# Kernel tuning notes

Measured on AMD Instinct MI355X. Metric: run time of the kernel, lower is better.

Reference implementation:

```python
import jax, jax.numpy as jnp
import numpy as np

NUM_HEADS = 12


def _build_mask(N, unseen_size, dtype):
    # Columns for the last `unseen_size` tokens are masked (-inf) for every
    # query row EXCEPT the diagonal entries in that block (each unseen token
    # may attend to itself). Matches the original Python-loop construction.
    idx = jnp.arange(N)
    col_unseen = idx[None, :] >= (N - unseen_size)
    off_diag = idx[:, None] != idx[None, :]
    return jnp.where(col_unseen & off_diag, -jnp.inf, jnp.asarray(0.0, dtype))


def reference(x, w_qkv, w_proj, b_proj, unseen_size):
    B, N, C = x.shape
    H = NUM_HEADS
    d = C // H
    scale = d ** -0.5
    # qkv: (B,N,3C) -> (3,B,H,N,d)
    qkv = (x @ w_qkv.T).reshape(B, N, 3, H, d).transpose(2, 0, 3, 1, 4)
    q, k, v = qkv[0], qkv[1], qkv[2]
    attn = jnp.einsum('bhqd,bhkd->bhqk', q, k) * scale
    attn = attn + _build_mask(N, unseen_size, attn.dtype)  # broadcast (N,N)
    attn = jax.nn.softmax(attn, axis=-1)
    out = jnp.einsum('bhqk,bhkd->bhqd', attn, v)
    out = out.transpose(0, 2, 1, 3).reshape(B, N, C)
    return out @ w_proj.T + b_proj


def setup_inputs() -> dict:
    key = jax.random.key(0)
    k1, k2, k3 = jax.random.split(key, 3)
    B, N, C = 2, 2048, 768
    x = jax.random.normal(k1, (B, N, C), dtype=jnp.float32)
    w_qkv = jax.random.normal(k2, (3 * C, C), dtype=jnp.float32) * (C ** -0.5)
    w_proj = jax.random.normal(k3, (C, C), dtype=jnp.float32) * (C ** -0.5)
    b_proj = jnp.zeros((C,), dtype=jnp.float32)
    return {"x": x, "w_qkv": w_qkv, "w_proj": w_proj, "b_proj": b_proj,
            "unseen_size": 512}
```

## Files before the change

kernel.cpp:

```cpp
#include <hip/hip_runtime.h>
#include <math.h>

#define NH 12
#define DH 64
#define NSEQ 2048
#define NB 2
#define CDIM 768
#define NVIS 1536

typedef _Float16 half8 __attribute__((ext_vector_type(8)));
typedef _Float16 half4 __attribute__((ext_vector_type(4)));
typedef float floatx4 __attribute__((ext_vector_type(4)));

static constexpr size_t SZ_X    = (size_t)NB*NSEQ*CDIM;
static constexpr size_t SZ_WQKV = (size_t)3*CDIM*CDIM;
static constexpr size_t SZ_WP   = (size_t)CDIM*CDIM;
static constexpr size_t SZ_HEAD = (size_t)NB*NH*NSEQ*DH;

__global__ __launch_bounds__(256) void convert_kernel(
    const float* __restrict__ x, const float* __restrict__ wqkv, const float* __restrict__ wp,
    _Float16* __restrict__ xb, _Float16* __restrict__ wqkvb, _Float16* __restrict__ wpb)
{
  size_t idx = ((size_t)blockIdx.x*256 + threadIdx.x)*4;
  const float* src; _Float16* dst; size_t off;
  if (idx < SZ_X)                        { src = x;    dst = xb;    off = idx; }
  else if (idx < SZ_X+SZ_WQKV)           { src = wqkv; dst = wqkvb; off = idx - SZ_X; }
  else if (idx < SZ_X+SZ_WQKV+SZ_WP)     { src = wp;   dst = wpb;   off = idx - SZ_X - SZ_WQKV; }
  else return;
  float4 v = *reinterpret_cast<const float4*>(src + off);
  _Float16 o[4] = {(_Float16)v.x,(_Float16)v.y,(_Float16)v.z,(_Float16)v.w};
  *reinterpret_cast<uint2*>(dst + off) = *reinterpret_cast<uint2*>(o);
}

template<int MODE>
__global__ __launch_bounds__(256) void gemm_bt(
    const _Float16* __restrict__ A, const _Float16* __restrict__ Bt,
    const float* __restrict__ bias,
    _Float16* __restrict__ qb, _Float16* __restrict__ kb, _Float16* __restrict__ vb,
    float* __restrict__ outp)
{
  constexpr int K = CDIM;
  constexpr int LDSST = 40;
  __shared__ _Float16 As[128*LDSST];
  __shared__ _Float16 Bs[128*LDSST];
  const int tid = threadIdx.x;
  const int lane = tid & 63, wid = tid >> 6;
  const int l15 = lane & 15, quad = lane >> 4;
  const int wm = (wid >> 1)*64, wn = (wid & 1)*64;
  const int tileN = blockIdx.x*128, tileM = blockIdx.y*128;
  const int srow = tid >> 2, scol = (tid & 3)*8;
  floatx4 acc[4][4] = {};
  for (int k0 = 0; k0 < K; k0 += 32) {
    uint4 a0 = *reinterpret_cast<const uint4*>(A  + (size_t)(tileM+srow)*K    + k0 + scol);
    uint4 a1 = *reinterpret_cast<const uint4*>(A  + (size_t)(tileM+64+srow)*K + k0 + scol);
    uint4 b0 = *reinterpret_cast<const uint4*>(Bt + (size_t)(tileN+srow)*K    + k0 + scol);
    uint4 b1 = *reinterpret_cast<const uint4*>(Bt + (size_t)(tileN+64+srow)*K + k0 + scol);
    __syncthreads();
    *reinterpret_cast<uint4*>(&As[srow*LDSST + scol])      = a0;
    *reinterpret_cast<uint4*>(&As[(64+srow)*LDSST + scol]) = a1;
    *reinterpret_cast<uint4*>(&Bs[srow*LDSST + scol])      = b0;
    *reinterpret_cast<uint4*>(&Bs[(64+srow)*LDSST + scol]) = b1;
    __syncthreads();
    half8 af[4], bfr[4];
    #pragma unroll
    for (int mi=0; mi<4; mi++)
      af[mi] = *reinterpret_cast<const half8*>(&As[(wm+mi*16+l15)*LDSST + quad*8]);
    #pragma unroll
    for (int ni=0; ni<4; ni++)
      bfr[ni] = *reinterpret_cast<const half8*>(&Bs[(wn+ni*16+l15)*LDSST + quad*8]);
    #pragma unroll
    for (int mi=0; mi<4; mi++)
      #pragma unroll
      for (int ni=0; ni<4; ni++)
        acc[mi][ni] = __builtin_amdgcn_mfma_f32_16x16x32_f16(af[mi], bfr[ni], acc[mi][ni], 0,0,0);
  }
  #pragma unroll
  for (int mi=0; mi<4; mi++)
    #pragma unroll
    for (int ni=0; ni<4; ni++) {
      int n = tileN + wn + ni*16 + l15;
      int m0 = tileM + wm + mi*16 + quad*4;
      if (MODE == 0) {
        int part = n / CDIM, rem = n - part*CDIM;
        int h = rem >> 6, dd = rem & 63;
        int b = m0 >> 11, i0 = m0 & 2047;
        if (part == 2) {
          half4 pk = {(_Float16)acc[mi][ni][0], (_Float16)acc[mi][ni][1],
                      (_Float16)acc[mi][ni][2], (_Float16)acc[mi][ni][3]};
          *reinterpret_cast<half4*>(&vb[(((size_t)b*NH + h)*DH + dd)*NSEQ + i0]) = pk;
        } else {
          _Float16* dst = part ? kb : qb;
          float sc = part ? 1.0f : 0.125f;
          #pragma unroll
          for (int r = 0; r < 4; r++)
            dst[(((size_t)b*NH + h)*NSEQ + i0 + r)*DH + dd] = (_Float16)(acc[mi][ni][r]*sc);
        }
      } else {
        #pragma unroll
        for (int r = 0; r < 4; r++)
          outp[(size_t)(m0 + r)*CDIM + n] = acc[mi][ni][r] + bias[n];
      }
    }
}

__global__ __launch_bounds__(256) void fa_kernel(
    const _Float16* __restrict__ qg, const _Float16* __restrict__ kg,
    const _Float16* __restrict__ vtg, _Float16* __restrict__ og)
{
  constexpr int LDK = 72;
  constexpr int LDP = 72;
  __shared__ _Float16 Ks[64*LDK];
  __shared__ _Float16 Vt[64*LDK];
  __shared__ _Float16 Ps[4][16*LDP];
  const int blk = blockIdx.x;
  const int idx = blk >> 3;
  const int bh = (blk & 7)*3 + (idx % 3);
  const int qbase = (idx / 3) * 64;
  const int tid = threadIdx.x;
  const int lane = tid & 63, w = tid >> 6;
  const int l15 = lane & 15, quad = lane >> 4;
  const _Float16* qptr = qg + ((size_t)bh*NSEQ + qbase + w*16 + l15)*DH + quad*8;
  half8 qf0 = *reinterpret_cast<const half8*>(qptr);
  half8 qf1 = *reinterpret_cast<const half8*>(qptr + 32);
  floatx4 o[4] = {};
  float lsum = 0.f;
  const int srow = tid >> 3, scol = (tid & 7)*8;
  const _Float16* kbp = kg  + (size_t)bh*NSEQ*DH;
  const _Float16* vbp = vtg + (size_t)bh*DH*NSEQ;
  for (int t = 0; t < 24; t++) {
    const int kvbase = t*64;
    const _Float16* kp = kbp + (size_t)(kvbase + srow)*DH + scol;
    const _Float16* vp = vbp + (size_t)srow*NSEQ + kvbase + scol;
    uint4 k0 = *reinterpret_cast<const uint4*>(kp);
    uint4 k1 = *reinterpret_cast<const uint4*>(kp + 32*DH);
    uint4 v0 = *reinterpret_cast<const uint4*>(vp);
    uint4 v1 = *reinterpret_cast<const uint4*>(vp + 32*NSEQ);
    __syncthreads();
    *reinterpret_cast<uint4*>(&Ks[srow*LDK + scol])      = k0;
    *reinterpret_cast<uint4*>(&Ks[(32+srow)*LDK + scol]) = k1;
    *reinterpret_cast<uint4*>(&Vt[srow*LDK + scol])      = v0;
    *reinterpret_cast<uint4*>(&Vt[(32+srow)*LDK + scol]) = v1;
    __syncthreads();
    #pragma unroll
    for (int f = 0; f < 4; f++) {
      half8 kf0 = *reinterpret_cast<const half8*>(&Ks[(f*16+l15)*LDK + quad*8]);
      half8 kf1 = *reinterpret_cast<const half8*>(&Ks[(f*16+l15)*LDK + 32 + quad*8]);
      floatx4 st = {};
      st = __builtin_amdgcn_mfma_f32_16x16x32_f16(kf0, qf0, st, 0,0,0);
      st = __builtin_amdgcn_mfma_f32_16x16x32_f16(kf1, qf1, st, 0,0,0);
      float e0 = __expf(st[0]), e1 = __expf(st[1]), e2 = __expf(st[2]), e3 = __expf(st[3]);
      lsum += (e0+e1)+(e2+e3);
      half4 pk = {(_Float16)e0,(_Float16)e1,(_Float16)e2,(_Float16)e3};
      *reinterpret_cast<half4*>(&Ps[w][l15*LDP + f*16 + quad*4]) = pk;
    }
    half8 pb0 = *reinterpret_cast<const half8*>(&Ps[w][l15*LDP + quad*8]);
    half8 pb1 = *reinterpret_cast<const half8*>(&Ps[w][l15*LDP + 32 + quad*8]);
    #pragma unroll
    for (int df = 0; df < 4; df++) {
      half8 vf0 = *reinterpret_cast<const half8*>(&Vt[(df*16+l15)*LDK + quad*8]);
      half8 vf1 = *reinterpret_cast<const half8*>(&Vt[(df*16+l15)*LDK + 32 + quad*8]);
      o[df] = __builtin_amdgcn_mfma_f32_16x16x32_f16(vf0, pb0, o[df], 0,0,0);
      o[df] = __builtin_amdgcn_mfma_f32_16x16x32_f16(vf1, pb1, o[df], 0,0,0);
    }
  }
  if (qbase >= NVIS) {
    const _Float16* kp = kbp + (size_t)(qbase + w*16 + l15)*DH + quad*8;
    half8 kf0 = *reinterpret_cast<const half8*>(kp);
    half8 kf1 = *reinterpret_cast<const half8*>(kp + 32);
    float pd = 0.f;
    #pragma unroll
    for (int j = 0; j < 8; j++)
      pd += (float)qf0[j]*(float)kf0[j] + (float)qf1[j]*(float)kf1[j];
    pd += __shfl_xor(pd, 16);
    pd += __shfl_xor(pd, 32);
    float e = __expf(pd);
    lsum += 0.25f*e;
    #pragma unroll
    for (int df = 0; df < 4; df++)
      #pragma unroll
      for (int r = 0; r < 4; r++)
        o[df][r] += e * (float)vbp[(size_t)(df*16+quad*4+r)*NSEQ + qbase + w*16 + l15];
  }
  lsum += __shfl_xor(lsum, 16);
  lsum += __shfl_xor(lsum, 32);
  float inv = 1.0f / lsum;
  const int b = bh / NH, h = bh - b*NH;
  size_t obase = ((size_t)b*NSEQ + qbase + w*16 + l15)*CDIM + h*DH;
  #pragma unroll
  for (int df = 0; df < 4; df++) {
    half4 pk = {(_Float16)(o[df][0]*inv), (_Float16)(o[df][1]*inv),
                (_Float16)(o[df][2]*inv), (_Float16)(o[df][3]*inv)};
    *reinterpret_cast<half4*>(&og[obase + df*16 + quad*4]) = pk;
  }
}

extern "C" void kernel_launch(void* const* d_in, const int* in_sizes, int n_in,
                              void* d_out, int out_size, void* d_ws, size_t ws_size,
                              hipStream_t stream) {
  (void)in_sizes; (void)n_in; (void)out_size; (void)ws_size;
  const float* x     = (const float*)d_in[0];
  const float* wqkv  = (const float*)d_in[1];
  const float* wproj = (const float*)d_in[2];
  const float* bproj = (const float*)d_in[3];

  _Float16* xb    = (_Float16*)d_ws;
  _Float16* wqkvb = xb + SZ_X;
  _Float16* wpb   = wqkvb + SZ_WQKV;
  _Float16* qb    = wpb + SZ_WP;
  _Float16* kb    = qb + SZ_HEAD;
  _Float16* vb    = kb + SZ_HEAD;
  _Float16* ob    = vb + SZ_HEAD;
  float* outp = (float*)d_out;

  size_t total = SZ_X + SZ_WQKV + SZ_WP;
  int cblocks = (int)((total/4 + 255)/256);
  convert_kernel<<<cblocks, 256, 0, stream>>>(x, wqkv, wproj, xb, wqkvb, wpb);
  gemm_bt<0><<<dim3(3*CDIM/128, NB*NSEQ/128), 256, 0, stream>>>(xb, wqkvb, nullptr, qb, kb, vb, nullptr);
  fa_kernel<<<NB*NH*(NSEQ/64), 256, 0, stream>>>(qb, kb, vb, ob);
  gemm_bt<1><<<dim3(CDIM/128, NB*NSEQ/128), 256, 0, stream>>>(ob, wpb, bproj, nullptr, nullptr, nullptr, outp);
}
```

Measured before the change: 173.8 us.

## Restructure attention kernel so each wave owns a KV slice, registers hold K/V

The flash-attention kernel is reorganised so each wave loads its own 16-row slice of every K/V tile straight into registers, with a one-tile-ahead prefetch, and computes scores against all 64 queries in the block. This removes the K/V shared-memory staging. The exponentials are shared through one shared P buffer, and row sums are reduced across waves through shared memory at the end. It also folds log2(e) into the Q scale so exp2f replaces __expf, and sets a launch-bounds occupancy hint of 3. In exchange it adds two block-wide barriers per tile for the P exchange, and each wave now holds all Q fragments in registers.

```diff
diff --git a/kernel.cpp b/kernel.cpp
--- a/kernel.cpp
+++ b/kernel.cpp
@@ -90,7 +90,7 @@
           *reinterpret_cast<half4*>(&vb[(((size_t)b*NH + h)*DH + dd)*NSEQ + i0]) = pk;
         } else {
           _Float16* dst = part ? kb : qb;
-          float sc = part ? 1.0f : 0.125f;
+          float sc = part ? 1.0f : 0.125f*1.44269504f;
           #pragma unroll
           for (int r = 0; r < 4; r++)
             dst[(((size_t)b*NH + h)*NSEQ + i0 + r)*DH + dd] = (_Float16)(acc[mi][ni][r]*sc);
@@ -103,15 +103,13 @@
     }
 }
 
-__global__ __launch_bounds__(256) void fa_kernel(
+__global__ __launch_bounds__(256, 3) void fa_kernel(
     const _Float16* __restrict__ qg, const _Float16* __restrict__ kg,
     const _Float16* __restrict__ vtg, _Float16* __restrict__ og)
 {
-  constexpr int LDK = 72;
   constexpr int LDP = 72;
-  __shared__ _Float16 Ks[64*LDK];
-  __shared__ _Float16 Vt[64*LDK];
-  __shared__ _Float16 Ps[4][16*LDP];
+  __shared__ _Float16 Ps[64*LDP];
+  __shared__ float Ls[4*64];
   const int blk = blockIdx.x;
   const int idx = blk >> 3;
   const int bh = (blk & 7)*3 + (idx % 3);
@@ -119,78 +117,97 @@
   const int tid = threadIdx.x;
   const int lane = tid & 63, w = tid >> 6;
   const int l15 = lane & 15, quad = lane >> 4;
-  const _Float16* qptr = qg + ((size_t)bh*NSEQ + qbase + w*16 + l15)*DH + quad*8;
-  half8 qf0 = *reinterpret_cast<const half8*>(qptr);
-  half8 qf1 = *reinterpret_cast<const half8*>(qptr + 32);
-  floatx4 o[4] = {};
-  float lsum = 0.f;
-  const int srow = tid >> 3, scol = (tid & 7)*8;
+  const _Float16* qp  = qg  + (size_t)bh*NSEQ*DH;
   const _Float16* kbp = kg  + (size_t)bh*NSEQ*DH;
   const _Float16* vbp = vtg + (size_t)bh*DH*NSEQ;
+  half8 qf[4][2];
+  #pragma unroll
+  for (int g = 0; g < 4; g++)
+    #pragma unroll
+    for (int c = 0; c < 2; c++)
+      qf[g][c] = *reinterpret_cast<const half8*>(qp + (size_t)(qbase + g*16 + l15)*DH + c*32 + quad*8);
+  const _Float16* kRow = kbp + (size_t)(w*16 + l15)*DH + quad*8;
+  const _Float16* vRow = vbp + (size_t)(w*16 + l15)*NSEQ + quad*8;
+  half8 kc0 = *reinterpret_cast<const half8*>(kRow);
+  half8 kc1 = *reinterpret_cast<const half8*>(kRow + 32);
+  half8 vc0 = *reinterpret_cast<const half8*>(vRow);
+  half8 vc1 = *reinterpret_cast<const half8*>(vRow + 32);
+  floatx4 o[4] = {};
+  float lsum[4] = {0.f, 0.f, 0.f, 0.f};
   for (int t = 0; t < 24; t++) {
-    const int kvbase = t*64;
-    const _Float16* kp = kbp + (size_t)(kvbase + srow)*DH + scol;
-    const _Float16* vp = vbp + (size_t)srow*NSEQ + kvbase + scol;
-    uint4 k0 = *reinterpret_cast<const uint4*>(kp);
-    uint4 k1 = *reinterpret_cast<const uint4*>(kp + 32*DH);
-    uint4 v0 = *reinterpret_cast<const uint4*>(vp);
-    uint4 v1 = *reinterpret_cast<const uint4*>(vp + 32*NSEQ);
-    __syncthreads();
-    *reinterpret_cast<uint4*>(&Ks[srow*LDK + scol])      = k0;
-    *reinterpret_cast<uint4*>(&Ks[(32+srow)*LDK + scol]) = k1;
-    *reinterpret_cast<uint4*>(&Vt[srow*LDK + scol])      = v0;
-    *reinterpret_cast<uint4*>(&Vt[(32+srow)*LDK + scol]) = v1;
-    __syncthreads();
-    #pragma unroll
-    for (int f = 0; f < 4; f++) {
-      half8 kf0 = *reinterpret_cast<const half8*>(&Ks[(f*16+l15)*LDK + quad*8]);
-      half8 kf1 = *reinterpret_cast<const half8*>(&Ks[(f*16+l15)*LDK + 32 + quad*8]);
-      floatx4 st = {};
-      st = __builtin_amdgcn_mfma_f32_16x16x32_f16(kf0, qf0, st, 0,0,0);
-      st = __builtin_amdgcn_mfma_f32_16x16x32_f16(kf1, qf1, st, 0,0,0);
-      float e0 = __expf(st[0]), e1 = __expf(st[1]), e2 = __expf(st[2]), e3 = __expf(st[3]);
-      lsum += (e0+e1)+(e2+e3);
-      half4 pk = {(_Float16)e0,(_Float16)e1,(_Float16)e2,(_Float16)e3};
-      *reinterpret_cast<half4*>(&Ps[w][l15*LDP + f*16 + quad*4]) = pk;
-    }
-    half8 pb0 = *reinterpret_cast<const half8*>(&Ps[w][l15*LDP + quad*8]);
-    half8 pb1 = *reinterpret_cast<const half8*>(&Ps[w][l15*LDP + 32 + quad*8]);
-    #pragma unroll
-    for (int df = 0; df < 4; df++) {
-      half8 vf0 = *reinterpret_cast<const half8*>(&Vt[(df*16+l15)*LDK + quad*8]);
-      half8 vf1 = *reinterpret_cast<const half8*>(&Vt[(df*16+l15)*LDK + 32 + quad*8]);
-      o[df] = __builtin_amdgcn_mfma_f32_16x16x32_f16(vf0, pb0, o[df], 0,0,0);
-      o[df] = __builtin_amdgcn_mfma_f32_16x16x32_f16(vf1, pb1, o[df], 0,0,0);
-    }
-  }
+    const int tn = (t + 1 < 24) ? t + 1 : 0;
+    half8 kn0 = *reinterpret_cast<const half8*>(kRow + (size_t)tn*64*DH);
+    half8 kn1 = *reinterpret_cast<const half8*>(kRow + (size_t)tn*64*DH + 32);
+    half8 vn0 = *reinterpret_cast<const half8*>(vRow + tn*64);
+    half8 vn1 = *reinterpret_cast<const half8*>(vRow + tn*64 + 32);
+    floatx4 st[4] = {};
+    #pragma unroll
+    for (int g = 0; g < 4; g++) {
+      st[g] = __builtin_amdgcn_mfma_f32_16x16x32_f16(kc0, qf[g][0], st[g], 0,0,0);
+      st[g] = __builtin_amdgcn_mfma_f32_16x16x32_f16(kc1, qf[g][1], st[g], 0,0,0);
+    }
+    half4 pk[4];
+    #pragma unroll
+    for (int g = 0; g < 4; g++) {
+      float e0 = exp2f(st[g][0]), e1 = exp2f(st[g][1]);
+      float e2 = exp2f(st[g][2]), e3 = exp2f(st[g][3]);
+      lsum[g] += (e0+e1)+(e2+e3);
+      pk[g] = half4{(_Float16)e0,(_Float16)e1,(_Float16)e2,(_Float16)e3};
+    }
+    __syncthreads();
+    #pragma unroll
+    for (int g = 0; g < 4; g++)
+      *reinterpret_cast<half4*>(&Ps[(g*16+l15)*LDP + w*16 + quad*4]) = pk[g];
+    __syncthreads();
+    #pragma unroll
+    for (int g = 0; g < 4; g++) {
+      half8 pb0 = *reinterpret_cast<const half8*>(&Ps[(g*16+l15)*LDP + quad*8]);
+      half8 pb1 = *reinterpret_cast<const half8*>(&Ps[(g*16+l15)*LDP + 32 + quad*8]);
+      o[g] = __builtin_amdgcn_mfma_f32_16x16x32_f16(vc0, pb0, o[g], 0,0,0);
+      o[g] = __builtin_amdgcn_mfma_f32_16x16x32_f16(vc1, pb1, o[g], 0,0,0);
+    }
+    kc0 = kn0; kc1 = kn1; vc0 = vn0; vc1 = vn1;
+  }
+  #pragma unroll
+  for (int g = 0; g < 4; g++) {
+    lsum[g] += __shfl_xor(lsum[g], 16);
+    lsum[g] += __shfl_xor(lsum[g], 32);
+  }
+  if (lane < 16) {
+    #pragma unroll
+    for (int g = 0; g < 4; g++) Ls[w*64 + g*16 + lane] = lsum[g];
+  }
+  __syncthreads();
+  float den[4];
+  #pragma unroll
+  for (int g = 0; g < 4; g++)
+    den[g] = Ls[g*16+l15] + Ls[64+g*16+l15] + Ls[128+g*16+l15] + Ls[192+g*16+l15];
   if (qbase >= NVIS) {
-    const _Float16* kp = kbp + (size_t)(qbase + w*16 + l15)*DH + quad*8;
-    half8 kf0 = *reinterpret_cast<const half8*>(kp);
-    half8 kf1 = *reinterpret_cast<const half8*>(kp + 32);
-    float pd = 0.f;
-    #pragma unroll
-    for (int j = 0; j < 8; j++)
-      pd += (float)qf0[j]*(float)kf0[j] + (float)qf1[j]*(float)kf1[j];
-    pd += __shfl_xor(pd, 16);
-    pd += __shfl_xor(pd, 32);
-    float e = __expf(pd);
-    lsum += 0.25f*e;
-    #pragma unroll
-    for (int df = 0; df < 4; df++)
+    #pragma unroll
+    for (int g = 0; g < 4; g++) {
+      half8 kd0 = *reinterpret_cast<const half8*>(kbp + (size_t)(qbase + g*16 + l15)*DH + quad*8);
+      half8 kd1 = *reinterpret_cast<const half8*>(kbp + (size_t)(qbase + g*16 + l15)*DH + 32 + quad*8);
+      float pd = 0.f;
+      #pragma unroll
+      for (int j = 0; j < 8; j++)
+        pd += (float)qf[g][0][j]*(float)kd0[j] + (float)qf[g][1][j]*(float)kd1[j];
+      pd += __shfl_xor(pd, 16);
+      pd += __shfl_xor(pd, 32);
+      float e = exp2f(pd);
+      den[g] += e;
       #pragma unroll
       for (int r = 0; r < 4; r++)
-        o[df][r] += e * (float)vbp[(size_t)(df*16+quad*4+r)*NSEQ + qbase + w*16 + l15];
-  }
-  lsum += __shfl_xor(lsum, 16);
-  lsum += __shfl_xor(lsum, 32);
-  float inv = 1.0f / lsum;
+        o[g][r] += e * (float)vbp[(size_t)(w*16+quad*4+r)*NSEQ + qbase + g*16 + l15];
+    }
+  }
   const int b = bh / NH, h = bh - b*NH;
-  size_t obase = ((size_t)b*NSEQ + qbase + w*16 + l15)*CDIM + h*DH;
-  #pragma unroll
-  for (int df = 0; df < 4; df++) {
-    half4 pk = {(_Float16)(o[df][0]*inv), (_Float16)(o[df][1]*inv),
-                (_Float16)(o[df][2]*inv), (_Float16)(o[df][3]*inv)};
-    *reinterpret_cast<half4*>(&og[obase + df*16 + quad*4]) = pk;
+  #pragma unroll
+  for (int g = 0; g < 4; g++) {
+    float inv = 1.0f / den[g];
+    half4 pk = {(_Float16)(o[g][0]*inv), (_Float16)(o[g][1]*inv),
+                (_Float16)(o[g][2]*inv), (_Float16)(o[g][3]*inv)};
+    size_t oaddr = ((size_t)b*NSEQ + qbase + g*16 + l15)*CDIM + h*DH + w*16 + quad*4;
+    *reinterpret_cast<half4*>(&og[oaddr]) = pk;
   }
 }
 
```

After: 176.4 us. About the same (+1.5%).
